# Performance work log

Hardware: AMD Instinct MI355X
Metric: run time of the kernel (lower is better)

## Reference

```python
import jax, jax.numpy as jnp
import numpy as np

PAD = float(-2**32 + 1)


def setup_inputs() -> dict:
    key = jax.random.key(0)
    ks = jax.random.split(key, 10)
    B, S, D = 8, 1024, 1024
    s = 0.02  # keep projections in sane range
    return {
        "Q": jax.random.normal(ks[0], (B, S, D), jnp.float32),
        "K": jax.random.normal(ks[1], (B, S, D), jnp.float32),
        "V": jax.random.normal(ks[2], (B, S, D), jnp.float32),
        "WQ": jax.random.normal(ks[3], (D, D), jnp.float32) * s,
        "bQ": jnp.zeros((D,), jnp.float32),
        "WK": jax.random.normal(ks[4], (D, D), jnp.float32) * s,
        "bK": jnp.zeros((D,), jnp.float32),
        "WV": jax.random.normal(ks[5], (D, D), jnp.float32) * s,
        "bV": jnp.zeros((D,), jnp.float32),
        "WO": jax.random.normal(ks[6], (D, D), jnp.float32) * s,
        "bO": jnp.zeros((D,), jnp.float32),
        "h": 16,
    }


def reference(Q, K, V, WQ, bQ, WK, bK, WV, bV, WO, bO, h):
    B, S, D = Q.shape
    dk = D // h
    # Dense projections with relu activation (as in the Keras layer)
    Qp = jax.nn.relu(Q @ WQ + bQ)
    Kp = jax.nn.relu(K @ WK + bK)
    Vp = jax.nn.relu(V @ WV + bV)
    # tf.concat(tf.split(x, h, axis=2), axis=0): head-major stacking -> (h, B, S, dk)
    qh = Qp.reshape(B, S, h, dk).transpose(2, 0, 1, 3)
    kh = Kp.reshape(B, S, h, dk).transpose(2, 0, 1, 3)
    vh = Vp.reshape(B, S, h, dk).transpose(2, 0, 1, 3)
    # scaled dot product; NOTE: source scales by 1/sqrt(d_model), not 1/sqrt(d_k)
    scores = jnp.einsum('hbqd,hbkd->hbqk', qh, kh) / jnp.sqrt(jnp.float32(D))
    # key padding mask: zero key rows -> large negative
    kmask = jnp.sum(jnp.abs(kh), axis=-1) != 0  # (h,B,Tk)
    scores = jnp.where(kmask[:, :, None, :], scores, PAD)
    w = jax.nn.softmax(scores, axis=-1)
    # query padding mask: zero query rows -> zero weights
    qmask = jnp.sign(jnp.sum(jnp.abs(qh), axis=-1))  # (h,B,Tq), 0/1
    w = w * qmask[:, :, :, None]
    # dropout_prob = 0.0 -> identity
    out = jnp.einsum('hbqk,hbkd->hbqd', w, vh)
    # tf.concat(tf.split(dot_product, h, axis=0), axis=2) -> (B,S,h*dk)
    out = out.transpose(1, 2, 0, 3).reshape(B, S, D)
    return jax.nn.relu(out @ WO + bO)
```

## Files before the change

### kernel.cpp

```cpp
#include <hip/hip_runtime.h>
#include <hip/hip_bf16.h>
#include <cstdint>

#define DEV __device__ __forceinline__

typedef __attribute__((ext_vector_type(4))) float f32x4;
typedef __attribute__((ext_vector_type(8))) short b16x8;
typedef __attribute__((ext_vector_type(4))) unsigned short u16x4;
typedef __attribute__((ext_vector_type(8))) unsigned short u16x8;
typedef __attribute__((ext_vector_type(2))) unsigned int u32x2;
typedef __attribute__((ext_vector_type(4))) unsigned int u32x4;

typedef __attribute__((address_space(1))) void gvoid_t;
typedef __attribute__((address_space(3))) void lvoid_t;

static constexpr int Bsz = 8, Ssz = 1024, Dsz = 1024;
static constexpr int Mrows = Bsz * Ssz;

DEV void gld16(const void* g, void* l) {
  __builtin_amdgcn_global_load_lds((gvoid_t*)(uintptr_t)g,
                                   (lvoid_t*)(unsigned)(uintptr_t)l, 16, 0, 0);
}

DEV unsigned short f2bf(float x) {
  unsigned int u = __float_as_uint(x);
  u += 0x7fffu + ((u >> 16) & 1u);
  return (unsigned short)(u >> 16);
}

DEV unsigned int cvt2(float lo, float hi) {
  __hip_bfloat162 h = __float22bfloat162_rn(make_float2(lo, hi));
  unsigned int u;
  __builtin_memcpy(&u, &h, 4);
  return u;
}

DEV float fexp2(float x) {
#if __has_builtin(__builtin_amdgcn_exp2f)
  return __builtin_amdgcn_exp2f(x);
#else
  return exp2f(x);
#endif
}

__global__ __launch_bounds__(256) void wconv_kernel(
    const float* __restrict__ WQ, const float* __restrict__ WK,
    const float* __restrict__ WV, const float* __restrict__ WO,
    unsigned short* __restrict__ Wt) {
  __shared__ float tile[64][65];
  const int w = blockIdx.z;
  const float* W = (w == 0) ? WQ : (w == 1) ? WK : (w == 2) ? WV : WO;
  const int k0 = blockIdx.x * 64, n0 = blockIdx.y * 64;
  const int t = threadIdx.x;
  {
    const int r = t >> 4;
    const int c = (t & 15) * 4;
#pragma unroll
    for (int i = 0; i < 4; ++i) {
      f32x4 v = *(const f32x4*)(W + (size_t)(k0 + i * 16 + r) * Dsz + n0 + c);
      tile[i * 16 + r][c + 0] = v[0];
      tile[i * 16 + r][c + 1] = v[1];
      tile[i * 16 + r][c + 2] = v[2];
      tile[i * 16 + r][c + 3] = v[3];
    }
  }
  __syncthreads();
  {
    const int n = t >> 2;
    const int ks = (t & 3) * 16;
    unsigned short* dst =
        Wt + (size_t)w * Dsz * Dsz + (size_t)(n0 + n) * Dsz + k0 + ks;
#pragma unroll
    for (int j = 0; j < 16; j += 4) {
      u16x4 p;
#pragma unroll
      for (int jj = 0; jj < 4; ++jj) p[jj] = f2bf(tile[ks + j + jj][n]);
      *(u16x4*)(dst + j) = p;
    }
  }
}

template <int OUT_MODE>
DEV void gemm_body_f32(unsigned short* __restrict__ Asl,
                       unsigned short* __restrict__ Bsl,
                       const float* __restrict__ A,
                       const unsigned short* __restrict__ Bt,
                       const float* __restrict__ bias, void* __restrict__ C_,
                       int m0, int n0, float outscale) {
  constexpr int Kd = 1024, Nd = 1024;
  const int t = threadIdx.x, lane = t & 63, wave = t >> 6;
  const int grp = lane >> 4, r16 = lane & 15;
  const int wm = wave >> 2, wn = wave & 3;
  const int swz = (r16 & 7) << 4;
  f32x4 acc[4][4] = {};
  f32x4 areg[2][2];

  auto loadA = [&](int kt) {
#pragma unroll
    for (int it = 0; it < 2; ++it) {
      int chunk = it * 512 + t;
      int row = chunk >> 3, c = chunk & 7;
      int csw = c ^ (row & 7);
      const float* src = A + (size_t)(m0 + row) * Kd + kt + csw * 8;
      areg[it][0] = *(const f32x4*)src;
      areg[it][1] = *(const f32x4*)(src + 4);
    }
  };
  auto writeA = [&]() {
#pragma unroll
    for (int it = 0; it < 2; ++it) {
      int chunk = it * 512 + t;
      u32x4 w;
      w[0] = cvt2(areg[it][0][0], areg[it][0][1]);
      w[1] = cvt2(areg[it][0][2], areg[it][0][3]);
      w[2] = cvt2(areg[it][1][0], areg[it][1][1]);
      w[3] = cvt2(areg[it][1][2], areg[it][1][3]);
      *(u32x4*)((char*)Asl + chunk * 16) = w;
    }
  };
  auto stageB = [&](int kt, int pb) {
#pragma unroll
    for (int j = 0; j < 4; ++j) {
      int chunk = (wave * 4 + j) * 64 + lane;
      int row = chunk >> 3, c = chunk & 7;
      int csw = c ^ (row & 7);
      gld16(Bt + (size_t)(n0 + row) * Kd + kt + csw * 8,
            (char*)Bsl + pb * 32768 + (wave * 4 + j) * 1024);
    }
  };

  loadA(0);
  stageB(0, 0);
  int cur = 0;
  for (int kt = 0; kt < Kd; kt += 64) {
    writeA();
    __syncthreads();
    if (kt < Kd - 64) {
      stageB(kt + 64, cur ^ 1);
      loadA(kt + 64);
    }
#pragma unroll
    for (int cs = 0; cs < 2; ++cs) {
      b16x8 af[4], bfr[4];
#pragma unroll
      for (int mi = 0; mi < 4; ++mi)
        af[mi] = *(const b16x8*)((char*)Asl + (wm * 64 + mi * 16 + r16) * 128 +
                                 ((cs * 64 + grp * 16) ^ swz));
#pragma unroll
      for (int ni = 0; ni < 4; ++ni)
        bfr[ni] = *(const b16x8*)((char*)Bsl + cur * 32768 +
                                  (wn * 64 + ni * 16 + r16) * 128 +
                                  ((cs * 64 + grp * 16) ^ swz));
#pragma unroll
      for (int mi = 0; mi < 4; ++mi)
#pragma unroll
        for (int ni = 0; ni < 4; ++ni)
          acc[mi][ni] = __builtin_amdgcn_mfma_f32_16x16x32_bf16(
              af[mi], bfr[ni], acc[mi][ni], 0, 0, 0);
    }
    asm volatile("s_waitcnt lgkmcnt(0)" ::: "memory");
    __builtin_amdgcn_s_barrier();
    __builtin_amdgcn_sched_barrier(0);
    cur ^= 1;
  }
#pragma unroll
  for (int mi = 0; mi < 4; ++mi) {
#pragma unroll
    for (int ni = 0; ni < 4; ++ni) {
      int col = n0 + wn * 64 + ni * 16 + r16;
      float bv = bias[col];
      int row0 = m0 + wm * 64 + mi * 16 + grp * 4;
      if constexpr (OUT_MODE == 2) {
        int bb = row0 >> 10, s = row0 & 1023;
        u16x4 pk;
#pragma unroll
        for (int r = 0; r < 4; ++r)
          pk[r] = f2bf(fmaxf(acc[mi][ni][r] + bv, 0.0f) * outscale);
        *(u16x4*)((unsigned short*)C_ +
                  (((size_t)(bb * 1024 + col)) << 10) + s) = pk;
      } else {
#pragma unroll
        for (int r = 0; r < 4; ++r) {
          float v = fmaxf(acc[mi][ni][r] + bv, 0.0f) * outscale;
          ((unsigned short*)C_)[(size_t)(row0 + r) * Nd + col] = f2bf(v);
        }
      }
    }
  }
}

DEV void gemm_body_bf16(unsigned short* __restrict__ Asl,
                        unsigned short* __restrict__ Bsl,
                        const unsigned short* __restrict__ A,
                        const unsigned short* __restrict__ Bt,
                        const float* __restrict__ bias, float* __restrict__ C_,
                        int m0, int n0) {
  constexpr int Kd = 1024, Nd = 1024;
  const int t = threadIdx.x, lane = t & 63, wave = t >> 6;
  const int grp = lane >> 4, r16 = lane & 15;
  const int wm = wave >> 1, wn = wave & 1;
  const int swz = (r16 & 7) << 4;
  f32x4 acc[4][4] = {};
  for (int kt = 0; kt < Kd; kt += 64) {
#pragma unroll
    for (int j = 0; j < 4; ++j) {
      int chunk = (wave * 4 + j) * 64 + lane;
      int row = chunk >> 3, c = chunk & 7;
      int csw = c ^ (row & 7);
      gld16(Bt + (size_t)(n0 + row) * Kd + kt + csw * 8,
            (char*)Bsl + (wave * 4 + j) * 1024);
      gld16(A + (size_t)(m0 + row) * Kd + kt + csw * 8,
            (char*)Asl + (wave * 4 + j) * 1024);
    }
    __syncthreads();
#pragma unroll
    for (int cs = 0; cs < 2; ++cs) {
      b16x8 af[4], bfr[4];
#pragma unroll
      for (int mi = 0; mi < 4; ++mi)
        af[mi] = *(const b16x8*)((char*)Asl + (wm * 64 + mi * 16 + r16) * 128 +
                                 ((cs * 64 + grp * 16) ^ swz));
#pragma unroll
      for (int ni = 0; ni < 4; ++ni)
        bfr[ni] = *(const b16x8*)((char*)Bsl + (wn * 64 + ni * 16 + r16) * 128 +
                                  ((cs * 64 + grp * 16) ^ swz));
#pragma unroll
      for (int mi = 0; mi < 4; ++mi)
#pragma unroll
        for (int ni = 0; ni < 4; ++ni)
          acc[mi][ni] = __builtin_amdgcn_mfma_f32_16x16x32_bf16(
              af[mi], bfr[ni], acc[mi][ni], 0, 0, 0);
    }
    __syncthreads();
  }
#pragma unroll
  for (int mi = 0; mi < 4; ++mi) {
#pragma unroll
    for (int ni = 0; ni < 4; ++ni) {
      int col = n0 + wn * 64 + ni * 16 + r16;
      float bv = bias[col];
      int row0 = m0 + wm * 64 + mi * 16 + grp * 4;
#pragma unroll
      for (int r = 0; r < 4; ++r) {
        float v = fmaxf(acc[mi][ni][r] + bv, 0.0f);
        C_[(size_t)(row0 + r) * Nd + col] = v;
      }
    }
  }
}

static constexpr float QSCALE = 0.03125f * 1.4426950408889634f;

__global__ __launch_bounds__(512) void proj3_kernel(
    const float* __restrict__ Q, const float* __restrict__ K,
    const float* __restrict__ V, const unsigned short* __restrict__ Wt,
    const float* __restrict__ bQ, const float* __restrict__ bK,
    const float* __restrict__ bV, unsigned short* __restrict__ Qp,
    unsigned short* __restrict__ Kp, unsigned short* __restrict__ VpT) {
  __shared__ unsigned short Asl[128 * 64] __attribute__((aligned(16)));
  __shared__ unsigned short Bsl[2 * 256 * 64] __attribute__((aligned(16)));
  const size_t DD = (size_t)Dsz * Dsz;
  const int bid = blockIdx.x;
  const int id2 = (bid & 7) * 32 + (bid >> 3);
  const int n0 = (id2 & 3) * 256, m0 = (id2 >> 2) * 128;
  const int z = blockIdx.z;
  if (z == 0)
    gemm_body_f32<1>(Asl, Bsl, Q, Wt, bQ, Qp, m0, n0, QSCALE);
  else if (z == 1)
    gemm_body_f32<1>(Asl, Bsl, K, Wt + DD, bK, Kp, m0, n0, 1.0f);
  else
    gemm_body_f32<2>(Asl, Bsl, V, Wt + 2 * DD, bV, VpT, m0, n0, 1.0f);
}

__global__ __launch_bounds__(256) void out_gemm_kernel(
    const unsigned short* __restrict__ AO,
    const unsigned short* __restrict__ WOt, const float* __restrict__ bO,
    float* __restrict__ Out) {
  __shared__ unsigned short Asl[128 * 64] __attribute__((aligned(16)));
  __shared__ unsigned short Bsl[128 * 64] __attribute__((aligned(16)));
  const int bid = blockIdx.x;
  const int id2 = (bid & 7) * 64 + (bid >> 3);
  const int n0 = (id2 & 7) * 128, m0 = (id2 >> 3) * 128;
  gemm_body_bf16(Asl, Bsl, AO, WOt, bO, Out, m0, n0);
}

__global__ __launch_bounds__(512, 4) void attn_kernel(
    const unsigned short* __restrict__ Qp, const unsigned short* __restrict__ Kp,
    const unsigned short* __restrict__ VpT, unsigned short* __restrict__ AO) {
  __shared__ unsigned short Ks[2][64 * 64] __attribute__((aligned(16)));
  __shared__ unsigned short Vs[2][64 * 64] __attribute__((aligned(16)));
  __shared__ unsigned short Ps[16][16 * 64] __attribute__((aligned(16)));
  const int t = threadIdx.x, lane = t & 63, wave = t >> 6;
  const int grp = lane >> 4, r16 = lane & 15;
  const int bid = blockIdx.x;
  const int id2 = (bid & 7) * 64 + (bid >> 3);
  const int q0 = (id2 & 3) * 256;
  const int bh = id2 >> 2;
  const int b = bh & 7, head = bh >> 3;

  const int srow = t >> 3, scc = t & 7;
  const int csw = scc ^ (srow & 7);
  const unsigned short* kbase = Kp + ((size_t)b * Ssz) * Dsz + head * 64;
  const unsigned short* vbase = VpT + ((size_t)b * Dsz + head * 64) * Ssz;

  const int sqA = q0 + wave * 16 + r16;
  const unsigned short* qbA = Qp + ((size_t)b * Ssz + sqA) * Dsz + head * 64;
  const unsigned short* qbB = qbA + (size_t)128 * Dsz;
  b16x8 qfA0 = *(const b16x8*)(qbA + grp * 8);
  b16x8 qfA1 = *(const b16x8*)(qbA + 32 + grp * 8);
  b16x8 qfB0 = *(const b16x8*)(qbB + grp * 8);
  b16x8 qfB1 = *(const b16x8*)(qbB + 32 + grp * 8);

  f32x4 oA[4] = {}, oB[4] = {};
  f32x4 olA = {}, olB = {};
  const f32x4 zero4 = {0.0f, 0.0f, 0.0f, 0.0f};
  const b16x8 ones = {16256, 16256, 16256, 16256,
                      16256, 16256, 16256, 16256};

  auto stage = [&](int kv0, int pb) {
    gld16(kbase + (size_t)(kv0 + srow) * Dsz + csw * 8,
          (char*)Ks[pb] + wave * 1024);
    gld16(vbase + (size_t)srow * Ssz + kv0 + csw * 8,
          (char*)Vs[pb] + wave * 1024);
  };

  stage(0, 0);
  __syncthreads();
  int cur = 0;

  for (int it = 0; it < 16; ++it) {
    if (it < 15) stage((it + 1) * 64, cur ^ 1);

    __builtin_amdgcn_s_setprio(1);
    f32x4 scA[4], scB[4];
#pragma unroll
    for (int f = 0; f < 4; ++f) {
      int k = f * 16 + r16;
      int kswz = (k & 7) << 4;
      const char* kb = (const char*)Ks[cur] + k * 128;
      b16x8 kf0 = *(const b16x8*)(kb + ((grp * 16) ^ kswz));
      b16x8 kf1 = *(const b16x8*)(kb + ((64 + grp * 16) ^ kswz));
      f32x4 sA = __builtin_amdgcn_mfma_f32_16x16x32_bf16(kf0, qfA0, zero4, 0, 0, 0);
      scA[f] = __builtin_amdgcn_mfma_f32_16x16x32_bf16(kf1, qfA1, sA, 0, 0, 0);
      f32x4 sB = __builtin_amdgcn_mfma_f32_16x16x32_bf16(kf0, qfB0, zero4, 0, 0, 0);
      scB[f] = __builtin_amdgcn_mfma_f32_16x16x32_bf16(kf1, qfB1, sB, 0, 0, 0);
    }
    __builtin_amdgcn_s_setprio(0);

    {
      int qs = (r16 & 7) << 4;
      char* prowA = (char*)Ps + (wave * 2 + 0) * 2048 + r16 * 128;
      char* prowB = (char*)Ps + (wave * 2 + 1) * 2048 + r16 * 128;
#pragma unroll
      for (int f = 0; f < 4; ++f) {
        u32x2 w;
        w[0] = cvt2(fexp2(scA[f][0]), fexp2(scA[f][1]));
        w[1] = cvt2(fexp2(scA[f][2]), fexp2(scA[f][3]));
        *(u32x2*)(prowA + ((f * 32 + grp * 8) ^ qs)) = w;
      }
#pragma unroll
      for (int f = 0; f < 4; ++f) {
        u32x2 w;
        w[0] = cvt2(fexp2(scB[f][0]), fexp2(scB[f][1]));
        w[1] = cvt2(fexp2(scB[f][2]), fexp2(scB[f][3]));
        *(u32x2*)(prowB + ((f * 32 + grp * 8) ^ qs)) = w;
      }
    }

    __builtin_amdgcn_s_setprio(1);
#pragma unroll
    for (int ks = 0; ks < 2; ++ks) {
      int pswz = (r16 & 7) << 4;
      int poff = r16 * 128 + ((ks * 64 + grp * 16) ^ pswz);
      b16x8 paA = *(const b16x8*)((char*)Ps + (wave * 2 + 0) * 2048 + poff);
      b16x8 paB = *(const b16x8*)((char*)Ps + (wave * 2 + 1) * 2048 + poff);
      olA = __builtin_amdgcn_mfma_f32_16x16x32_bf16(paA, ones, olA, 0, 0, 0);
      olB = __builtin_amdgcn_mfma_f32_16x16x32_bf16(paB, ones, olB, 0, 0, 0);
#pragma unroll
      for (int fc = 0; fc < 4; ++fc) {
        int d = fc * 16 + r16;
        int vswz = (d & 7) << 4;
        b16x8 vb = *(const b16x8*)((char*)Vs[cur] + d * 128 +
                                   ((ks * 64 + grp * 16) ^ vswz));
        oA[fc] = __builtin_amdgcn_mfma_f32_16x16x32_bf16(paA, vb, oA[fc], 0, 0, 0);
        oB[fc] = __builtin_amdgcn_mfma_f32_16x16x32_bf16(paB, vb, oB[fc], 0, 0, 0);
      }
    }
    __builtin_amdgcn_s_setprio(0);
    __syncthreads();
    cur ^= 1;
  }

#pragma unroll
  for (int fc = 0; fc < 4; ++fc) {
    int col = head * 64 + fc * 16 + r16;
#pragma unroll
    for (int r = 0; r < 4; ++r) {
      int rowA = q0 + wave * 16 + grp * 4 + r;
      AO[((size_t)b * Ssz + rowA) * Dsz + col] = f2bf(oA[fc][r] / olA[r]);
      AO[((size_t)b * Ssz + rowA + 128) * Dsz + col] = f2bf(oB[fc][r] / olB[r]);
    }
  }
}

extern "C" void kernel_launch(void* const* d_in, const int* in_sizes, int n_in,
                              void* d_out, int out_size, void* d_ws,
                              size_t ws_size, hipStream_t stream) {
  const float* Q = (const float*)d_in[0];
  const float* K = (const float*)d_in[1];
  const float* V = (const float*)d_in[2];
  const float* WQ = (const float*)d_in[3];
  const float* bQ = (const float*)d_in[4];
  const float* WK = (const float*)d_in[5];
  const float* bK = (const float*)d_in[6];
  const float* WV = (const float*)d_in[7];
  const float* bV = (const float*)d_in[8];
  const float* WO = (const float*)d_in[9];
  const float* bO = (const float*)d_in[10];

  char* ws = (char*)d_ws;
  const size_t MB = 1024ull * 1024ull;
  const size_t DD = (size_t)Dsz * Dsz;
  unsigned short* Wt = (unsigned short*)(ws);
  unsigned short* Qp = (unsigned short*)(ws + 8 * MB);
  unsigned short* Kp = (unsigned short*)(ws + 24 * MB);
  unsigned short* VpT = (unsigned short*)(ws + 40 * MB);
  unsigned short* AO = (unsigned short*)(ws + 56 * MB);

  wconv_kernel<<<dim3(16, 16, 4), 256, 0, stream>>>(WQ, WK, WV, WO, Wt);
  proj3_kernel<<<dim3(256, 1, 3), 512, 0, stream>>>(Q, K, V, Wt, bQ, bK, bV,
                                                    Qp, Kp, VpT);
  attn_kernel<<<512, 512, 0, stream>>>(Qp, Kp, VpT, AO);
  out_gemm_kernel<<<512, 256, 0, stream>>>(AO, Wt + 3 * DD, bO, (float*)d_out);
}
```

Baseline: 152.6 us.

## Reuse pipelined 128x256 GEMM body for output projection

The output-projection GEMM drops its simple single-buffered body (128x128 tiles, 256 threads, global_load_lds for both operands, two barriers per k-step). It now uses the same templated body as the input projections: 512 threads, 128x256 tiles, register-prefetched A and double-buffered B in LDS. A new bf16 A path copies the loaded registers straight to LDS, and a float output mode is added. The goal is more overlap of loads with MFMA and more reuse per tile, at the cost of a grid of 256 blocks, which may underfill the GPU's compute units.

```diff
diff --git a/kernel.cpp b/kernel.cpp
--- a/kernel.cpp
+++ b/kernel.cpp
@@ -80,20 +80,21 @@
   }
 }
 
-template <int OUT_MODE>
-DEV void gemm_body_f32(unsigned short* __restrict__ Asl,
-                       unsigned short* __restrict__ Bsl,
-                       const float* __restrict__ A,
-                       const unsigned short* __restrict__ Bt,
-                       const float* __restrict__ bias, void* __restrict__ C_,
-                       int m0, int n0, float outscale) {
+template <bool A_BF16, int OUT_MODE>
+DEV void gemm_body(unsigned short* __restrict__ Asl,
+                   unsigned short* __restrict__ Bsl,
+                   const void* __restrict__ A_,
+                   const unsigned short* __restrict__ Bt,
+                   const float* __restrict__ bias, void* __restrict__ C_,
+                   int m0, int n0, float outscale) {
   constexpr int Kd = 1024, Nd = 1024;
   const int t = threadIdx.x, lane = t & 63, wave = t >> 6;
   const int grp = lane >> 4, r16 = lane & 15;
   const int wm = wave >> 2, wn = wave & 3;
   const int swz = (r16 & 7) << 4;
   f32x4 acc[4][4] = {};
-  f32x4 areg[2][2];
+  f32x4 aregf[2][2];
+  u32x4 aregb[2];
 
   auto loadA = [&](int kt) {
 #pragma unroll
@@ -101,21 +102,31 @@
       int chunk = it * 512 + t;
       int row = chunk >> 3, c = chunk & 7;
       int csw = c ^ (row & 7);
-      const float* src = A + (size_t)(m0 + row) * Kd + kt + csw * 8;
-      areg[it][0] = *(const f32x4*)src;
-      areg[it][1] = *(const f32x4*)(src + 4);
+      if constexpr (A_BF16) {
+        const unsigned short* A = (const unsigned short*)A_;
+        aregb[it] = *(const u32x4*)(A + (size_t)(m0 + row) * Kd + kt + csw * 8);
+      } else {
+        const float* A = (const float*)A_;
+        const float* src = A + (size_t)(m0 + row) * Kd + kt + csw * 8;
+        aregf[it][0] = *(const f32x4*)src;
+        aregf[it][1] = *(const f32x4*)(src + 4);
+      }
     }
   };
   auto writeA = [&]() {
 #pragma unroll
     for (int it = 0; it < 2; ++it) {
       int chunk = it * 512 + t;
-      u32x4 w;
-      w[0] = cvt2(areg[it][0][0], areg[it][0][1]);
-      w[1] = cvt2(areg[it][0][2], areg[it][0][3]);
-      w[2] = cvt2(areg[it][1][0], areg[it][1][1]);
-      w[3] = cvt2(areg[it][1][2], areg[it][1][3]);
-      *(u32x4*)((char*)Asl + chunk * 16) = w;
+      if constexpr (A_BF16) {
+        *(u32x4*)((char*)Asl + chunk * 16) = aregb[it];
+      } else {
+        u32x4 w;
+        w[0] = cvt2(aregf[it][0][0], aregf[it][0][1]);
+        w[1] = cvt2(aregf[it][0][2], aregf[it][0][3]);
+        w[2] = cvt2(aregf[it][1][0], aregf[it][1][1]);
+        w[3] = cvt2(aregf[it][1][2], aregf[it][1][3]);
+        *(u32x4*)((char*)Asl + chunk * 16) = w;
+      }
     }
   };
   auto stageB = [&](int kt, int pb) {
@@ -182,68 +193,11 @@
 #pragma unroll
         for (int r = 0; r < 4; ++r) {
           float v = fmaxf(acc[mi][ni][r] + bv, 0.0f) * outscale;
-          ((unsigned short*)C_)[(size_t)(row0 + r) * Nd + col] = f2bf(v);
+          if constexpr (OUT_MODE == 1)
+            ((unsigned short*)C_)[(size_t)(row0 + r) * Nd + col] = f2bf(v);
+          else
+            ((float*)C_)[(size_t)(row0 + r) * Nd + col] = v;
         }
-      }
-    }
-  }
-}
-
-DEV void gemm_body_bf16(unsigned short* __restrict__ Asl,
-                        unsigned short* __restrict__ Bsl,
-                        const unsigned short* __restrict__ A,
-                        const unsigned short* __restrict__ Bt,
-                        const float* __restrict__ bias, float* __restrict__ C_,
-                        int m0, int n0) {
-  constexpr int Kd = 1024, Nd = 1024;
-  const int t = threadIdx.x, lane = t & 63, wave = t >> 6;
-  const int grp = lane >> 4, r16 = lane & 15;
-  const int wm = wave >> 1, wn = wave & 1;
-  const int swz = (r16 & 7) << 4;
-  f32x4 acc[4][4] = {};
-  for (int kt = 0; kt < Kd; kt += 64) {
-#pragma unroll
-    for (int j = 0; j < 4; ++j) {
-      int chunk = (wave * 4 + j) * 64 + lane;
-      int row = chunk >> 3, c = chunk & 7;
-      int csw = c ^ (row & 7);
-      gld16(Bt + (size_t)(n0 + row) * Kd + kt + csw * 8,
-            (char*)Bsl + (wave * 4 + j) * 1024);
-      gld16(A + (size_t)(m0 + row) * Kd + kt + csw * 8,
-            (char*)Asl + (wave * 4 + j) * 1024);
-    }
-    __syncthreads();
-#pragma unroll
-    for (int cs = 0; cs < 2; ++cs) {
-      b16x8 af[4], bfr[4];
-#pragma unroll
-      for (int mi = 0; mi < 4; ++mi)
-        af[mi] = *(const b16x8*)((char*)Asl + (wm * 64 + mi * 16 + r16) * 128 +
-                                 ((cs * 64 + grp * 16) ^ swz));
-#pragma unroll
-      for (int ni = 0; ni < 4; ++ni)
-        bfr[ni] = *(const b16x8*)((char*)Bsl + (wn * 64 + ni * 16 + r16) * 128 +
-                                  ((cs * 64 + grp * 16) ^ swz));
-#pragma unroll
-      for (int mi = 0; mi < 4; ++mi)
-#pragma unroll
-        for (int ni = 0; ni < 4; ++ni)
-          acc[mi][ni] = __builtin_amdgcn_mfma_f32_16x16x32_bf16(
-              af[mi], bfr[ni], acc[mi][ni], 0, 0, 0);
-    }
-    __syncthreads();
-  }
-#pragma unroll
-  for (int mi = 0; mi < 4; ++mi) {
-#pragma unroll
-    for (int ni = 0; ni < 4; ++ni) {
-      int col = n0 + wn * 64 + ni * 16 + r16;
-      float bv = bias[col];
-      int row0 = m0 + wm * 64 + mi * 16 + grp * 4;
-#pragma unroll
-      for (int r = 0; r < 4; ++r) {
-        float v = fmaxf(acc[mi][ni][r] + bv, 0.0f);
-        C_[(size_t)(row0 + r) * Nd + col] = v;
       }
     }
   }
@@ -265,23 +219,23 @@
   const int n0 = (id2 & 3) * 256, m0 = (id2 >> 2) * 128;
   const int z = blockIdx.z;
   if (z == 0)
-    gemm_body_f32<1>(Asl, Bsl, Q, Wt, bQ, Qp, m0, n0, QSCALE);
+    gemm_body<false, 1>(Asl, Bsl, Q, Wt, bQ, Qp, m0, n0, QSCALE);
   else if (z == 1)
-    gemm_body_f32<1>(Asl, Bsl, K, Wt + DD, bK, Kp, m0, n0, 1.0f);
+    gemm_body<false, 1>(Asl, Bsl, K, Wt + DD, bK, Kp, m0, n0, 1.0f);
   else
-    gemm_body_f32<2>(Asl, Bsl, V, Wt + 2 * DD, bV, VpT, m0, n0, 1.0f);
-}
-
-__global__ __launch_bounds__(256) void out_gemm_kernel(
+    gemm_body<false, 2>(Asl, Bsl, V, Wt + 2 * DD, bV, VpT, m0, n0, 1.0f);
+}
+
+__global__ __launch_bounds__(512) void out_gemm_kernel(
     const unsigned short* __restrict__ AO,
     const unsigned short* __restrict__ WOt, const float* __restrict__ bO,
     float* __restrict__ Out) {
   __shared__ unsigned short Asl[128 * 64] __attribute__((aligned(16)));
-  __shared__ unsigned short Bsl[128 * 64] __attribute__((aligned(16)));
+  __shared__ unsigned short Bsl[2 * 256 * 64] __attribute__((aligned(16)));
   const int bid = blockIdx.x;
-  const int id2 = (bid & 7) * 64 + (bid >> 3);
-  const int n0 = (id2 & 7) * 128, m0 = (id2 >> 3) * 128;
-  gemm_body_bf16(Asl, Bsl, AO, WOt, bO, Out, m0, n0);
+  const int id2 = (bid & 7) * 32 + (bid >> 3);
+  const int n0 = (id2 & 3) * 256, m0 = (id2 >> 2) * 128;
+  gemm_body<true, 0>(Asl, Bsl, AO, WOt, bO, Out, m0, n0, 1.0f);
 }
 
 __global__ __launch_bounds__(512, 4) void attn_kernel(
@@ -431,5 +385,5 @@
   proj3_kernel<<<dim3(256, 1, 3), 512, 0, stream>>>(Q, K, V, Wt, bQ, bK, bV,
                                                     Qp, Kp, VpT);
   attn_kernel<<<512, 512, 0, stream>>>(Qp, Kp, VpT, AO);
-  out_gemm_kernel<<<512, 256, 0, stream>>>(AO, Wt + 3 * DD, bO, (float*)d_out);
-}
+  out_gemm_kernel<<<256, 512, 0, stream>>>(AO, Wt + 3 * DD, bO, (float*)d_out);
+}
```

Result: no change. 150.7 us (median of 2 runs) (-1.2%).

## Prefetch A two k-steps ahead in projection GEMM and pipeline output GEMM

Applied to the files above, without the earlier changes.

The projection GEMM now keeps two register sets of fp32 A tiles, so global loads for step k+2 are issued while step k computes, and the loop is unrolled by two over the B double buffer. The output GEMM switches from a single-buffered 128x128 tile with 256 threads to the same 128x256, 512-thread, double-buffered B pipeline with register-staged A. The aim is to hide global load latency and cut the number of barriers per tile. In exchange it raises register pressure in the projection kernel, and the output GEMM launches fewer, larger blocks.

```diff
diff --git a/kernel.cpp b/kernel.cpp
--- a/kernel.cpp
+++ b/kernel.cpp
@@ -93,29 +93,136 @@
   const int wm = wave >> 2, wn = wave & 3;
   const int swz = (r16 & 7) << 4;
   f32x4 acc[4][4] = {};
-  f32x4 areg[2][2];
-
-  auto loadA = [&](int kt) {
+  f32x4 af0[2][2], af1[2][2];
+
+  auto loadA = [&](int kt, f32x4(&ar)[2][2]) {
 #pragma unroll
     for (int it = 0; it < 2; ++it) {
       int chunk = it * 512 + t;
       int row = chunk >> 3, c = chunk & 7;
       int csw = c ^ (row & 7);
       const float* src = A + (size_t)(m0 + row) * Kd + kt + csw * 8;
-      areg[it][0] = *(const f32x4*)src;
-      areg[it][1] = *(const f32x4*)(src + 4);
-    }
-  };
-  auto writeA = [&]() {
+      ar[it][0] = *(const f32x4*)src;
+      ar[it][1] = *(const f32x4*)(src + 4);
+    }
+  };
+  auto writeA = [&](f32x4(&ar)[2][2]) {
 #pragma unroll
     for (int it = 0; it < 2; ++it) {
       int chunk = it * 512 + t;
       u32x4 w;
-      w[0] = cvt2(areg[it][0][0], areg[it][0][1]);
-      w[1] = cvt2(areg[it][0][2], areg[it][0][3]);
-      w[2] = cvt2(areg[it][1][0], areg[it][1][1]);
-      w[3] = cvt2(areg[it][1][2], areg[it][1][3]);
+      w[0] = cvt2(ar[it][0][0], ar[it][0][1]);
+      w[1] = cvt2(ar[it][0][2], ar[it][0][3]);
+      w[2] = cvt2(ar[it][1][0], ar[it][1][1]);
+      w[3] = cvt2(ar[it][1][2], ar[it][1][3]);
       *(u32x4*)((char*)Asl + chunk * 16) = w;
+    }
+  };
+  auto stageB = [&](int kt, int pb) {
+#pragma unroll
+    for (int j = 0; j < 4; ++j) {
+      int chunk = (wave * 4 + j) * 64 + lane;
+      int row = chunk >> 3, c = chunk & 7;
+      int csw = c ^ (row & 7);
+      gld16(Bt + (size_t)(n0 + row) * Kd + kt + csw * 8,
+            (char*)Bsl + pb * 32768 + (wave * 4 + j) * 1024);
+    }
+  };
+  auto mfmaStep = [&](int pb) {
+#pragma unroll
+    for (int cs = 0; cs < 2; ++cs) {
+      b16x8 af[4], bfr[4];
+#pragma unroll
+      for (int mi = 0; mi < 4; ++mi)
+        af[mi] = *(const b16x8*)((char*)Asl + (wm * 64 + mi * 16 + r16) * 128 +
+                                 ((cs * 64 + grp * 16) ^ swz));
+#pragma unroll
+      for (int ni = 0; ni < 4; ++ni)
+        bfr[ni] = *(const b16x8*)((char*)Bsl + pb * 32768 +
+                                  (wn * 64 + ni * 16 + r16) * 128 +
+                                  ((cs * 64 + grp * 16) ^ swz));
+#pragma unroll
+      for (int mi = 0; mi < 4; ++mi)
+#pragma unroll
+        for (int ni = 0; ni < 4; ++ni)
+          acc[mi][ni] = __builtin_amdgcn_mfma_f32_16x16x32_bf16(
+              af[mi], bfr[ni], acc[mi][ni], 0, 0, 0);
+    }
+    asm volatile("s_waitcnt lgkmcnt(0)" ::: "memory");
+    __builtin_amdgcn_s_barrier();
+    __builtin_amdgcn_sched_barrier(0);
+  };
+
+  loadA(0, af0);
+  stageB(0, 0);
+  loadA(64, af1);
+
+  for (int kt0 = 0; kt0 < Kd; kt0 += 128) {
+    writeA(af0);
+    __syncthreads();
+    stageB(kt0 + 64, 1);
+    if (kt0 + 128 < Kd) loadA(kt0 + 128, af0);
+    mfmaStep(0);
+    writeA(af1);
+    __syncthreads();
+    if (kt0 + 128 < Kd) stageB(kt0 + 128, 0);
+    if (kt0 + 192 < Kd) loadA(kt0 + 192, af1);
+    mfmaStep(1);
+  }
+#pragma unroll
+  for (int mi = 0; mi < 4; ++mi) {
+#pragma unroll
+    for (int ni = 0; ni < 4; ++ni) {
+      int col = n0 + wn * 64 + ni * 16 + r16;
+      float bv = bias[col];
+      int row0 = m0 + wm * 64 + mi * 16 + grp * 4;
+      if constexpr (OUT_MODE == 2) {
+        int bb = row0 >> 10, s = row0 & 1023;
+        u16x4 pk;
+#pragma unroll
+        for (int r = 0; r < 4; ++r)
+          pk[r] = f2bf(fmaxf(acc[mi][ni][r] + bv, 0.0f) * outscale);
+        *(u16x4*)((unsigned short*)C_ +
+                  (((size_t)(bb * 1024 + col)) << 10) + s) = pk;
+      } else {
+#pragma unroll
+        for (int r = 0; r < 4; ++r) {
+          float v = fmaxf(acc[mi][ni][r] + bv, 0.0f) * outscale;
+          ((unsigned short*)C_)[(size_t)(row0 + r) * Nd + col] = f2bf(v);
+        }
+      }
+    }
+  }
+}
+
+DEV void gemm_body_bf16(unsigned short* __restrict__ Asl,
+                        unsigned short* __restrict__ Bsl,
+                        const unsigned short* __restrict__ A,
+                        const unsigned short* __restrict__ Bt,
+                        const float* __restrict__ bias, float* __restrict__ C_,
+                        int m0, int n0) {
+  constexpr int Kd = 1024, Nd = 1024;
+  const int t = threadIdx.x, lane = t & 63, wave = t >> 6;
+  const int grp = lane >> 4, r16 = lane & 15;
+  const int wm = wave >> 2, wn = wave & 3;
+  const int swz = (r16 & 7) << 4;
+  f32x4 acc[4][4] = {};
+  u32x4 aregb[2];
+
+  auto loadA = [&](int kt) {
+#pragma unroll
+    for (int it = 0; it < 2; ++it) {
+      int chunk = it * 512 + t;
+      int row = chunk >> 3, c = chunk & 7;
+      int csw = c ^ (row & 7);
+      aregb[it] = *(const u32x4*)(A + (size_t)(m0 + row) * Kd + kt + csw * 8);
+    }
+  };
+  auto writeA = [&]() {
+#pragma unroll
+    for (int it = 0; it < 2; ++it) {
+      int chunk = it * 512 + t;
+      *(u32x4*)((char*)Asl + chunk * 16) = aregb[it];
     }
   };
   auto stageB = [&](int kt, int pb) {
@@ -162,76 +269,6 @@
     __builtin_amdgcn_s_barrier();
     __builtin_amdgcn_sched_barrier(0);
     cur ^= 1;
-  }
-#pragma unroll
-  for (int mi = 0; mi < 4; ++mi) {
-#pragma unroll
-    for (int ni = 0; ni < 4; ++ni) {
-      int col = n0 + wn * 64 + ni * 16 + r16;
-      float bv = bias[col];
-      int row0 = m0 + wm * 64 + mi * 16 + grp * 4;
-      if constexpr (OUT_MODE == 2) {
-        int bb = row0 >> 10, s = row0 & 1023;
-        u16x4 pk;
-#pragma unroll
-        for (int r = 0; r < 4; ++r)
-          pk[r] = f2bf(fmaxf(acc[mi][ni][r] + bv, 0.0f) * outscale);
-        *(u16x4*)((unsigned short*)C_ +
-                  (((size_t)(bb * 1024 + col)) << 10) + s) = pk;
-      } else {
-#pragma unroll
-        for (int r = 0; r < 4; ++r) {
-          float v = fmaxf(acc[mi][ni][r] + bv, 0.0f) * outscale;
-          ((unsigned short*)C_)[(size_t)(row0 + r) * Nd + col] = f2bf(v);
-        }
-      }
-    }
-  }
-}
-
-DEV void gemm_body_bf16(unsigned short* __restrict__ Asl,
-                        unsigned short* __restrict__ Bsl,
-                        const unsigned short* __restrict__ A,
-                        const unsigned short* __restrict__ Bt,
-                        const float* __restrict__ bias, float* __restrict__ C_,
-                        int m0, int n0) {
-  constexpr int Kd = 1024, Nd = 1024;
-  const int t = threadIdx.x, lane = t & 63, wave = t >> 6;
-  const int grp = lane >> 4, r16 = lane & 15;
-  const int wm = wave >> 1, wn = wave & 1;
-  const int swz = (r16 & 7) << 4;
-  f32x4 acc[4][4] = {};
-  for (int kt = 0; kt < Kd; kt += 64) {
-#pragma unroll
-    for (int j = 0; j < 4; ++j) {
-      int chunk = (wave * 4 + j) * 64 + lane;
-      int row = chunk >> 3, c = chunk & 7;
-      int csw = c ^ (row & 7);
-      gld16(Bt + (size_t)(n0 + row) * Kd + kt + csw * 8,
-            (char*)Bsl + (wave * 4 + j) * 1024);
-      gld16(A + (size_t)(m0 + row) * Kd + kt + csw * 8,
-            (char*)Asl + (wave * 4 + j) * 1024);
-    }
-    __syncthreads();
-#pragma unroll
-    for (int cs = 0; cs < 2; ++cs) {
-      b16x8 af[4], bfr[4];
-#pragma unroll
-      for (int mi = 0; mi < 4; ++mi)
-        af[mi] = *(const b16x8*)((char*)Asl + (wm * 64 + mi * 16 + r16) * 128 +
-                                 ((cs * 64 + grp * 16) ^ swz));
-#pragma unroll
-      for (int ni = 0; ni < 4; ++ni)
-        bfr[ni] = *(const b16x8*)((char*)Bsl + (wn * 64 + ni * 16 + r16) * 128 +
-                                  ((cs * 64 + grp * 16) ^ swz));
-#pragma unroll
-      for (int mi = 0; mi < 4; ++mi)
-#pragma unroll
-        for (int ni = 0; ni < 4; ++ni)
-          acc[mi][ni] = __builtin_amdgcn_mfma_f32_16x16x32_bf16(
-              af[mi], bfr[ni], acc[mi][ni], 0, 0, 0);
-    }
-    __syncthreads();
   }
 #pragma unroll
   for (int mi = 0; mi < 4; ++mi) {
@@ -272,15 +309,15 @@
     gemm_body_f32<2>(Asl, Bsl, V, Wt + 2 * DD, bV, VpT, m0, n0, 1.0f);
 }
 
-__global__ __launch_bounds__(256) void out_gemm_kernel(
+__global__ __launch_bounds__(512) void out_gemm_kernel(
     const unsigned short* __restrict__ AO,
     const unsigned short* __restrict__ WOt, const float* __restrict__ bO,
     float* __restrict__ Out) {
   __shared__ unsigned short Asl[128 * 64] __attribute__((aligned(16)));
-  __shared__ unsigned short Bsl[128 * 64] __attribute__((aligned(16)));
+  __shared__ unsigned short Bsl[2 * 256 * 64] __attribute__((aligned(16)));
   const int bid = blockIdx.x;
-  const int id2 = (bid & 7) * 64 + (bid >> 3);
-  const int n0 = (id2 & 7) * 128, m0 = (id2 >> 3) * 128;
+  const int id2 = (bid & 7) * 32 + (bid >> 3);
+  const int n0 = (id2 & 3) * 256, m0 = (id2 >> 2) * 128;
   gemm_body_bf16(Asl, Bsl, AO, WOt, bO, Out, m0, n0);
 }
 
@@ -431,5 +468,5 @@
   proj3_kernel<<<dim3(256, 1, 3), 512, 0, stream>>>(Q, K, V, Wt, bQ, bK, bV,
                                                     Qp, Kp, VpT);
   attn_kernel<<<512, 512, 0, stream>>>(Qp, Kp, VpT, AO);
-  out_gemm_kernel<<<512, 256, 0, stream>>>(AO, Wt + 3 * DD, bO, (float*)d_out);
-}
+  out_gemm_kernel<<<256, 512, 0, stream>>>(AO, Wt + 3 * DD, bO, (float*)d_out);
+}
```

New measurement: 157.7 us. +3.4%, slower.
